# Kernel tuning notes

Measured on AMD Instinct MI355X. Metric: run time of the kernel, lower is better.

## Reference

```python
import jax, jax.numpy as jnp
import numpy as np
from jax import lax

T, D_IN, N = 8192, 1024, 1024


def setup_inputs() -> dict:
    key = jax.random.key(0)
    ks = jax.random.split(key, 8)
    s = 0.1  # truncated_normal stddev in original
    return {
        "x": jax.random.normal(ks[0], (T, D_IN), jnp.float32),
        # input projections (FullConnectLayer weights + biases)
        "Wx": jax.random.normal(ks[1], (D_IN, N), jnp.float32) * s,
        "bx": jnp.zeros((N,), jnp.float32),
        "Wu": jax.random.normal(ks[2], (D_IN, N), jnp.float32) * s,
        "bu": jnp.zeros((N,), jnp.float32),
        "Wr": jax.random.normal(ks[3], (D_IN, N), jnp.float32) * s,
        "br": jnp.zeros((N,), jnp.float32),
        # recurrent weights/biases
        "hW": jax.random.normal(ks[4], (N, N), jnp.float32) * s,
        "hUW": jax.random.normal(ks[5], (N, N), jnp.float32) * s,
        "hRW": jax.random.normal(ks[6], (N, N), jnp.float32) * s,
        "hB": jnp.zeros((N,), jnp.float32),
        "hUB": jnp.zeros((N,), jnp.float32),
        "hRB": jnp.zeros((N,), jnp.float32),
        # initial hidden state h (tf.Variable zeros [1, nNodes])
        "h0": jnp.zeros((1, N), jnp.float32),
    }


def reference(x, Wx, bx, Wu, bu, Wr, br, hW, hUW, hRW, hB, hUB, hRB, h0):
    # Precompute input-side gate projections for all timesteps (as original
    # does: xTransform/xUpdates/xResets are built once on the full sequence).
    xT = x @ Wx + bx  # [T, N] candidate input
    xU = x @ Wu + bu  # [T, N] update gate input
    xR = x @ Wr + br  # [T, N] reset gate input

    def step(h, xs):  # h: [N]
        xt, xu, xr = xs
        u = jax.nn.sigmoid(xu + h @ hUW + hUB)
        r = jax.nn.sigmoid(xr + h @ hRW + hRB)
        hc = jnp.tanh(xt + (r * h) @ hW + hB)
        # NOTE: faithful to original bug: (1-u)*hc + u*hc == hc
        h_new = (1.0 - u) * hc + u * hc
        return h_new, h_new

    _, hs = lax.scan(step, h0[0], (xT, xU, xR))
    return hs  # [T, N] == hStates.concat() since each state is [1, N]
```

## Files before the change

### kernel.cpp

```cpp
#include <hip/hip_runtime.h>
#include <hip/hip_bf16.h>
#include <math.h>

#define T_STEPS 8192
#define NN      1024
#define KWG     32
#define RT      512

typedef float f32x4 __attribute__((ext_vector_type(4)));

#define REP16(X) X(0) X(1) X(2) X(3) X(4) X(5) X(6) X(7) \
                 X(8) X(9) X(10) X(11) X(12) X(13) X(14) X(15)
#define REP8(X)  X(0) X(1) X(2) X(3) X(4) X(5) X(6) X(7)

__device__ __forceinline__ float fast_sigmoid(float z) {
    z = fminf(fmaxf(z, -30.f), 30.f);
    return 1.f / (1.f + __expf(-z));
}
__device__ __forceinline__ float fast_tanh(float x) {
    x = fminf(fmaxf(x, -9.f), 9.f);
    const float e = __expf(2.f * x);
    return (e - 1.f) / (e + 1.f);
}

__global__ __launch_bounds__(256) void gemm_bias(
    const float* __restrict__ A, const float* __restrict__ W,
    const float* __restrict__ bias, float* __restrict__ C)
{
    const int bn = blockIdx.x;
    const int bm = blockIdx.y;
    const int tid = threadIdx.x;

    __shared__ __align__(16) float As[16][68];
    __shared__ __align__(16) float Bs[16][68];

    const int row0 = bm * 64, col0 = bn * 64;
    const int tm = (tid >> 4) << 2;
    const int tn = (tid & 15) << 2;

    float acc[4][4] = {};

    for (int k0 = 0; k0 < 1024; k0 += 16) {
        {
            const int m = tid >> 2, kq = (tid & 3) << 2;
            const float4 v = *reinterpret_cast<const float4*>(&A[(size_t)(row0 + m) * 1024 + k0 + kq]);
            As[kq + 0][m] = v.x; As[kq + 1][m] = v.y; As[kq + 2][m] = v.z; As[kq + 3][m] = v.w;
            const int kk = tid >> 4, nq = (tid & 15) << 2;
            *reinterpret_cast<float4*>(&Bs[kk][nq]) =
                *reinterpret_cast<const float4*>(&W[(size_t)(k0 + kk) * 1024 + col0 + nq]);
        }
        __syncthreads();
#pragma unroll
        for (int k = 0; k < 16; ++k) {
            const float4 a4 = *reinterpret_cast<const float4*>(&As[k][tm]);
            const float4 b4 = *reinterpret_cast<const float4*>(&Bs[k][tn]);
            const float a[4] = {a4.x, a4.y, a4.z, a4.w};
            const float b[4] = {b4.x, b4.y, b4.z, b4.w};
#pragma unroll
            for (int i = 0; i < 4; ++i)
#pragma unroll
                for (int j = 0; j < 4; ++j) acc[i][j] += a[i] * b[j];
        }
        __syncthreads();
    }
#pragma unroll
    for (int i = 0; i < 4; ++i)
#pragma unroll
        for (int j = 0; j < 4; ++j)
            C[(size_t)(row0 + tm + i) * 1024 + col0 + tn + j] = acc[i][j] + bias[col0 + tn + j];
}

__global__ __launch_bounds__(RT, 1) void gru_rec(
    const float* __restrict__ xT, const float* __restrict__ xR,
    const float* __restrict__ hRW, const float* __restrict__ hW,
    const float* __restrict__ hRB, const float* __restrict__ hB,
    const float* __restrict__ h0, float* __restrict__ out,
    unsigned long long* __restrict__ P,
    unsigned long long* __restrict__ hbc)
{
    const int g = blockIdx.x;
    const int tid = threadIdx.x;
    const int lane = tid & 63;
    const int wave = tid >> 6;

    __shared__ __align__(16) float hsh[1088];
    __shared__ __align__(16) float rh[32];

    const int j = (wave << 2) | (lane >> 4);
    const int c = lane & 15;
    const bool leader1 = (c == 0);
    const int colj = g * 32 + j;

#define LD_W1(q) f32x4 w1_##q = { \
        hRW[(size_t)(c * 64 + 4 * q + 0) * NN + colj], \
        hRW[(size_t)(c * 64 + 4 * q + 1) * NN + colj], \
        hRW[(size_t)(c * 64 + 4 * q + 2) * NN + colj], \
        hRW[(size_t)(c * 64 + 4 * q + 3) * NN + colj] };
    REP16(LD_W1)

    const int n0 = tid, n1 = tid + RT;
    const int pi0 = n0 + (n0 >> 6) * 4, pi1 = n1 + (n1 >> 6) * 4;
#define LD_W2A(q) f32x4 w2a_##q = { \
        hW[(size_t)(g * 32 + 4 * q + 0) * NN + n0], \
        hW[(size_t)(g * 32 + 4 * q + 1) * NN + n0], \
        hW[(size_t)(g * 32 + 4 * q + 2) * NN + n0], \
        hW[(size_t)(g * 32 + 4 * q + 3) * NN + n0] };
    REP8(LD_W2A)
#define LD_W2B(q) f32x4 w2b_##q = { \
        hW[(size_t)(g * 32 + 4 * q + 0) * NN + n1], \
        hW[(size_t)(g * 32 + 4 * q + 1) * NN + n1], \
        hW[(size_t)(g * 32 + 4 * q + 2) * NN + n1], \
        hW[(size_t)(g * 32 + 4 * q + 3) * NN + n1] };
    REP8(LD_W2B)

#define PIN_W1(q)  asm volatile("" : "+v"(w1_##q));
#define PIN_W2A(q) asm volatile("" : "+v"(w2a_##q));
#define PIN_W2B(q) asm volatile("" : "+v"(w2b_##q));
    REP16(PIN_W1)
    REP8(PIN_W2A)
    REP8(PIN_W2B)

    const int jj = tid >> 4, cc = tid & 15;
    const int mjj = g * 32 + jj;
    const float hBo = hB[mjj];

    const int mj = colj;
    const int pij = mj + (mj >> 6) * 4;
    const float hRBj = hRB[mj];

    hsh[pi0] = h0[n0];
    hsh[pi1] = h0[n1];
    __syncthreads();

    float xr_n  = leader1   ? xR[mj]  : 0.f;
    float xto_n = (cc == 0) ? xT[mjj] : 0.f;

    for (int t = 0; t < T_STEPS; ++t) {
        const unsigned tag = (unsigned)(t + 1);
        unsigned long long* __restrict__ Pb = P   + (size_t)(t & 1) * KWG * NN;
        unsigned long long* __restrict__ Hb = hbc + (size_t)(t & 1) * NN;

        const float xr = xr_n, xto = xto_n;
        if (t + 1 < T_STEPS) {
            if (leader1) xr_n  = xR[(size_t)(t + 1) * NN + mj];
            if (cc == 0) xto_n = xT[(size_t)(t + 1) * NN + mjj];
        }

        f32x4 acc = {0.f, 0.f, 0.f, 0.f};
#define FMA_W1(q) { \
        const f32x4 hv = *reinterpret_cast<const f32x4*>(&hsh[c * 68 + 4 * q]); \
        acc += hv * w1_##q; }
        REP16(FMA_W1)
        float s = (acc.x + acc.y) + (acc.z + acc.w);
        s += __shfl_xor(s, 1); s += __shfl_xor(s, 2);
        s += __shfl_xor(s, 4); s += __shfl_xor(s, 8);
        if (leader1) rh[j] = fast_sigmoid(xr + hRBj + s) * hsh[pij];
        __syncthreads();

        f32x4 aa = {0.f, 0.f, 0.f, 0.f}, bb = {0.f, 0.f, 0.f, 0.f};
#define FMA_W2(q) { \
        const f32x4 rv = *reinterpret_cast<const f32x4*>(&rh[4 * q]); \
        aa += rv * w2a_##q; bb += rv * w2b_##q; }
        REP8(FMA_W2)
        const float p0 = (aa.x + aa.y) + (aa.z + aa.w);
        const float p1 = (bb.x + bb.y) + (bb.z + bb.w);
        __hip_atomic_store(&Pb[(size_t)g * NN + n0],
            ((unsigned long long)tag << 32) | (unsigned)__float_as_uint(p0),
            __ATOMIC_RELAXED, __HIP_MEMORY_SCOPE_AGENT);
        __hip_atomic_store(&Pb[(size_t)g * NN + n1],
            ((unsigned long long)tag << 32) | (unsigned)__float_as_uint(p1),
            __ATOMIC_RELAXED, __HIP_MEMORY_SCOPE_AGENT);

        float hn;
        {
            unsigned long long va = 0, vb = 0;
            bool fa = false, fb = false;
            do {
                if (!fa) { va = __hip_atomic_load(&Pb[(size_t)cc * NN + mjj],
                             __ATOMIC_RELAXED, __HIP_MEMORY_SCOPE_AGENT);
                           fa = ((unsigned)(va >> 32) == tag); }
                if (!fb) { vb = __hip_atomic_load(&Pb[(size_t)(cc + 16) * NN + mjj],
                             __ATOMIC_RELAXED, __HIP_MEMORY_SCOPE_AGENT);
                           fb = ((unsigned)(vb >> 32) == tag); }
            } while (!(fa && fb));
            float s2 = __uint_as_float((unsigned)va) + __uint_as_float((unsigned)vb);
            s2 += __shfl_xor(s2, 1); s2 += __shfl_xor(s2, 2);
            s2 += __shfl_xor(s2, 4); s2 += __shfl_xor(s2, 8);
            hn = fast_tanh(xto ? xto + s2 + hBo : s2 + hBo);
            hn = fast_tanh(__shfl(xto, (tid & ~15) & 63, 64) + s2 + hBo);
            if (cc == 0) {
                __hip_atomic_store(&Hb[mjj],
                    ((unsigned long long)tag << 32) | (unsigned)__float_as_uint(hn),
                    __ATOMIC_RELAXED, __HIP_MEMORY_SCOPE_AGENT);
            }
            if (cc == 1) out[(size_t)t * NN + mjj] = hn;
        }

        {
            unsigned long long ua = 0, ub = 0;
            bool fa = false, fb = false;
            do {
                if (!fa) { ua = __hip_atomic_load(&Hb[n0], __ATOMIC_RELAXED,
                             __HIP_MEMORY_SCOPE_AGENT);
                           fa = ((unsigned)(ua >> 32) == tag); }
                if (!fb) { ub = __hip_atomic_load(&Hb[n1], __ATOMIC_RELAXED,
                             __HIP_MEMORY_SCOPE_AGENT);
                           fb = ((unsigned)(ub >> 32) == tag); }
            } while (!(fa && fb));
            hsh[pi0] = __uint_as_float((unsigned)ua);
            hsh[pi1] = __uint_as_float((unsigned)ub);
        }
        __syncthreads();
    }
}

extern "C" void kernel_launch(void* const* d_in, const int* in_sizes, int n_in,
                              void* d_out, int out_size, void* d_ws, size_t ws_size,
                              hipStream_t stream) {
    const float* x   = (const float*)d_in[0];
    const float* Wx  = (const float*)d_in[1];
    const float* bx  = (const float*)d_in[2];
    const float* Wr  = (const float*)d_in[5];
    const float* br  = (const float*)d_in[6];
    const float* hW  = (const float*)d_in[7];
    const float* hRW = (const float*)d_in[9];
    const float* hB  = (const float*)d_in[10];
    const float* hRB = (const float*)d_in[12];
    const float* h0  = (const float*)d_in[13];
    float* out = (float*)d_out;

    char* ws = (char*)d_ws;
    float* xT = (float*)(ws);
    float* xR = (float*)(ws + 33554432);
    unsigned long long* P   = (unsigned long long*)(ws + 67108864);
    unsigned long long* hbc = (unsigned long long*)(ws + 67108864 + 524288);

    hipMemsetAsync(P, 0, (2 * KWG * NN + 2 * NN) * sizeof(unsigned long long), stream);

    gemm_bias<<<dim3(16, 128), 256, 0, stream>>>(x, Wx, bx, xT);
    gemm_bias<<<dim3(16, 128), 256, 0, stream>>>(x, Wr, br, xR);

    gru_rec<<<dim3(KWG), RT, 0, stream>>>(xT, xR, hRW, hW, hRB, hB, h0,
                                          out, P, hbc);
}
```

Measured before the change: 31.28 ms.

## Co-locate recurrent workgroups on one XCC and use non-coherent fast polling

Launches many workgroups and elects the 32 that land on one XCC (read from the hardware XCC id), so the per-step cross-workgroup exchange stays inside a single die's L2. Stores are written twice, once as a plain store and once as an agent-scope atomic, and polling first spins with sc0 loads before falling back to agent-scope atomic loads. The goal is to cut the latency of the per-timestep global handshake. It adds a startup election and barrier with a timeout, and depends on all 32 elected workgroups being resident at once. The fast path relies on cache-coherence behaviour that the code assumes rather than guarantees.

Measured after the change: 83.66 ms. 2.67x slower.

```diff
diff --git a/kernel.cpp b/kernel.cpp
--- a/kernel.cpp
+++ b/kernel.cpp
@@ -6,6 +6,8 @@
 #define NN      1024
 #define KWG     32
 #define RT      512
+#define NWG_LAUNCH 1024
+#define FAST_SPIN 24
 
 typedef float f32x4 __attribute__((ext_vector_type(4)));
 
@@ -21,6 +23,43 @@
     x = fminf(fmaxf(x, -9.f), 9.f);
     const float e = __expf(2.f * x);
     return (e - 1.f) / (e + 1.f);
+}
+
+__device__ __forceinline__ void st_2way(unsigned long long* p, unsigned long long v) {
+    asm volatile("global_store_dwordx2 %0, %1, off" :: "v"(p), "v"(v) : "memory");
+    __hip_atomic_store(p, v, __ATOMIC_RELAXED, __HIP_MEMORY_SCOPE_AGENT);
+}
+
+__device__ __forceinline__ bool poll2(const unsigned long long* pa,
+                                      const unsigned long long* pb,
+                                      unsigned tag, bool use_fast,
+                                      unsigned long long& va, unsigned long long& vb) {
+    bool fa = false, fb = false;
+    if (use_fast) {
+        for (int it = 0; it < FAST_SPIN; ++it) {
+            unsigned long long xa, xb;
+            asm volatile("global_load_dwordx2 %0, %2, off sc0\n\t"
+                         "global_load_dwordx2 %1, %3, off sc0\n\t"
+                         "s_waitcnt vmcnt(0)"
+                         : "=&v"(xa), "=&v"(xb) : "v"(pa), "v"(pb) : "memory");
+            if (!fa && (unsigned)(xa >> 32) == tag) { va = xa; fa = true; }
+            if (!fb && (unsigned)(xb >> 32) == tag) { vb = xb; fb = true; }
+            if (fa && fb) return true;
+        }
+    }
+    for (;;) {
+        if (!fa) {
+            const unsigned long long xa =
+                __hip_atomic_load(pa, __ATOMIC_RELAXED, __HIP_MEMORY_SCOPE_AGENT);
+            if ((unsigned)(xa >> 32) == tag) { va = xa; fa = true; }
+        }
+        if (!fb) {
+            const unsigned long long xb =
+                __hip_atomic_load(pb, __ATOMIC_RELAXED, __HIP_MEMORY_SCOPE_AGENT);
+            if ((unsigned)(xb >> 32) == tag) { vb = xb; fb = true; }
+        }
+        if (fa && fb) return false;
+    }
 }
 
 __global__ __launch_bounds__(256) void gemm_bias(
@@ -76,10 +115,29 @@
     const float* __restrict__ hRB, const float* __restrict__ hB,
     const float* __restrict__ h0, float* __restrict__ out,
     unsigned long long* __restrict__ P,
-    unsigned long long* __restrict__ hbc)
+    unsigned long long* __restrict__ hbc,
+    unsigned int* __restrict__ elect)
 {
-    const int g = blockIdx.x;
     const int tid = threadIdx.x;
+
+    __shared__ int s_g;
+    if (tid == 0) {
+        unsigned xcc;
+        asm volatile("s_getreg_b32 %0, hwreg(HW_REG_XCC_ID)" : "=s"(xcc));
+        xcc = (xcc & 0xfu) + 1u;
+        const unsigned old = atomicCAS(&elect[0], 0u, xcc);
+        const unsigned home = old ? old : xcc;
+        int slot = -1;
+        if (home == xcc) {
+            const unsigned s = atomicAdd(&elect[1], 1u);
+            if (s < KWG) slot = (int)s;
+        }
+        s_g = slot;
+    }
+    __syncthreads();
+    const int g = s_g;
+    if (g < 0) return;
+
     const int lane = tid & 63;
     const int wave = tid >> 6;
 
@@ -132,8 +190,18 @@
     hsh[pi1] = h0[n1];
     __syncthreads();
 
+    if (tid == 0) {
+        __hip_atomic_fetch_add(&elect[2], 1u, __ATOMIC_RELAXED, __HIP_MEMORY_SCOPE_AGENT);
+        const long long t0 = clock64();
+        while (__hip_atomic_load(&elect[2], __ATOMIC_RELAXED, __HIP_MEMORY_SCOPE_AGENT) < KWG
+               && (clock64() - t0) < (1LL << 22)) {}
+    }
+    __syncthreads();
+
     float xr_n  = leader1   ? xR[mj]  : 0.f;
     float xto_n = (cc == 0) ? xT[mjj] : 0.f;
+
+    bool fast1 = true, fast2 = true;
 
     for (int t = 0; t < T_STEPS; ++t) {
         const unsigned tag = (unsigned)(t + 1);
@@ -164,49 +232,32 @@
         REP8(FMA_W2)
         const float p0 = (aa.x + aa.y) + (aa.z + aa.w);
         const float p1 = (bb.x + bb.y) + (bb.z + bb.w);
-        __hip_atomic_store(&Pb[(size_t)g * NN + n0],
-            ((unsigned long long)tag << 32) | (unsigned)__float_as_uint(p0),
-            __ATOMIC_RELAXED, __HIP_MEMORY_SCOPE_AGENT);
-        __hip_atomic_store(&Pb[(size_t)g * NN + n1],
-            ((unsigned long long)tag << 32) | (unsigned)__float_as_uint(p1),
-            __ATOMIC_RELAXED, __HIP_MEMORY_SCOPE_AGENT);
-
-        float hn;
+        st_2way(&Pb[(size_t)g * NN + n0],
+                ((unsigned long long)tag << 32) | (unsigned)__float_as_uint(p0));
+        st_2way(&Pb[(size_t)g * NN + n1],
+                ((unsigned long long)tag << 32) | (unsigned)__float_as_uint(p1));
+
         {
             unsigned long long va = 0, vb = 0;
-            bool fa = false, fb = false;
-            do {
-                if (!fa) { va = __hip_atomic_load(&Pb[(size_t)cc * NN + mjj],
-                             __ATOMIC_RELAXED, __HIP_MEMORY_SCOPE_AGENT);
-                           fa = ((unsigned)(va >> 32) == tag); }
-                if (!fb) { vb = __hip_atomic_load(&Pb[(size_t)(cc + 16) * NN + mjj],
-                             __ATOMIC_RELAXED, __HIP_MEMORY_SCOPE_AGENT);
-                           fb = ((unsigned)(vb >> 32) == tag); }
-            } while (!(fa && fb));
+            const bool ff = poll2(&Pb[(size_t)cc * NN + mjj],
+                                  &Pb[(size_t)(cc + 16) * NN + mjj],
+                                  tag, fast1, va, vb);
+            fast1 = fast1 && ff;
             float s2 = __uint_as_float((unsigned)va) + __uint_as_float((unsigned)vb);
             s2 += __shfl_xor(s2, 1); s2 += __shfl_xor(s2, 2);
             s2 += __shfl_xor(s2, 4); s2 += __shfl_xor(s2, 8);
-            hn = fast_tanh(xto ? xto + s2 + hBo : s2 + hBo);
-            hn = fast_tanh(__shfl(xto, (tid & ~15) & 63, 64) + s2 + hBo);
             if (cc == 0) {
-                __hip_atomic_store(&Hb[mjj],
-                    ((unsigned long long)tag << 32) | (unsigned)__float_as_uint(hn),
-                    __ATOMIC_RELAXED, __HIP_MEMORY_SCOPE_AGENT);
+                const float hn = fast_tanh(xto + s2 + hBo);
+                st_2way(&Hb[mjj],
+                        ((unsigned long long)tag << 32) | (unsigned)__float_as_uint(hn));
+                out[(size_t)t * NN + mjj] = hn;
             }
-            if (cc == 1) out[(size_t)t * NN + mjj] = hn;
         }
 
         {
             unsigned long long ua = 0, ub = 0;
-            bool fa = false, fb = false;
-            do {
-                if (!fa) { ua = __hip_atomic_load(&Hb[n0], __ATOMIC_RELAXED,
-                             __HIP_MEMORY_SCOPE_AGENT);
-                           fa = ((unsigned)(ua >> 32) == tag); }
-                if (!fb) { ub = __hip_atomic_load(&Hb[n1], __ATOMIC_RELAXED,
-                             __HIP_MEMORY_SCOPE_AGENT);
-                           fb = ((unsigned)(ub >> 32) == tag); }
-            } while (!(fa && fb));
+            const bool ff = poll2(&Hb[n0], &Hb[n1], tag, fast2, ua, ub);
+            fast2 = fast2 && ff;
             hsh[pi0] = __uint_as_float((unsigned)ua);
             hsh[pi1] = __uint_as_float((unsigned)ub);
         }
@@ -232,14 +283,15 @@
     char* ws = (char*)d_ws;
     float* xT = (float*)(ws);
     float* xR = (float*)(ws + 33554432);
-    unsigned long long* P   = (unsigned long long*)(ws + 67108864);
-    unsigned long long* hbc = (unsigned long long*)(ws + 67108864 + 524288);
-
-    hipMemsetAsync(P, 0, (2 * KWG * NN + 2 * NN) * sizeof(unsigned long long), stream);
+    unsigned int* elect = (unsigned int*)(ws + 67108864);
+    unsigned long long* P   = (unsigned long long*)(ws + 67108864 + 4096);
+    unsigned long long* hbc = (unsigned long long*)(ws + 67108864 + 4096 + 524288);
+
+    hipMemsetAsync(ws + 67108864, 0, 4096 + 524288 + 16384, stream);
 
     gemm_bias<<<dim3(16, 128), 256, 0, stream>>>(x, Wx, bx, xT);
     gemm_bias<<<dim3(16, 128), 256, 0, stream>>>(x, Wr, br, xR);
 
-    gru_rec<<<dim3(KWG), RT, 0, stream>>>(xT, xR, hRW, hW, hRB, hB, h0,
-                                          out, P, hbc);
-}
+    gru_rec<<<dim3(NWG_LAUNCH), RT, 0, stream>>>(xT, xR, hRW, hW, hRB, hB, h0,
+                                                 out, P, hbc, elect);
+}
```

## Remove second grid-wide h broadcast by having every block reduce all partials redundantly

Applied to the files above, without the earlier changes.

Each block now gathers all 32 partial sums for the two hidden units each thread needs and applies tanh locally. This removes the separate hbc broadcast round and its second cross-block spin-wait per timestep. In exchange, global atomic-load traffic grows (32 loads per thread per step instead of 2) and the tanh is computed redundantly. The xT/xR prefetch for the next step is dropped in favour of direct loads at the current step.

After: 80.08 ms. 2.56x slower.

```diff
diff --git a/kernel.cpp b/kernel.cpp
--- a/kernel.cpp
+++ b/kernel.cpp
@@ -75,8 +75,7 @@
     const float* __restrict__ hRW, const float* __restrict__ hW,
     const float* __restrict__ hRB, const float* __restrict__ hB,
     const float* __restrict__ h0, float* __restrict__ out,
-    unsigned long long* __restrict__ P,
-    unsigned long long* __restrict__ hbc)
+    unsigned long long* __restrict__ P)
 {
     const int g = blockIdx.x;
     const int tid = threadIdx.x;
@@ -120,9 +119,8 @@
     REP8(PIN_W2A)
     REP8(PIN_W2B)
 
-    const int jj = tid >> 4, cc = tid & 15;
-    const int mjj = g * 32 + jj;
-    const float hBo = hB[mjj];
+    const float hB0 = hB[n0], hB1 = hB[n1];
+    const bool own0 = ((n0 >> 5) == g), own1 = ((n1 >> 5) == g);
 
     const int mj = colj;
     const int pij = mj + (mj >> 6) * 4;
@@ -132,19 +130,32 @@
     hsh[pi1] = h0[n1];
     __syncthreads();
 
-    float xr_n  = leader1   ? xR[mj]  : 0.f;
-    float xto_n = (cc == 0) ? xT[mjj] : 0.f;
+#define GATHER16(BASEPTR, SUMVAR, BIT) \
+    if (!(dmask & (BIT))) { \
+        unsigned long long v[16]; \
+        _Pragma("unroll") \
+        for (int q = 0; q < 16; ++q) \
+            v[q] = __hip_atomic_load((BASEPTR) + (size_t)q * NN, \
+                                     __ATOMIC_RELAXED, __HIP_MEMORY_SCOPE_AGENT); \
+        bool ok = true; \
+        _Pragma("unroll") \
+        for (int q = 0; q < 16; ++q) \
+            ok = ok && ((unsigned)(v[q] >> 32) == tag); \
+        if (ok) { \
+            float ssum = 0.f; \
+            _Pragma("unroll") \
+            for (int q = 0; q < 16; ++q) ssum += __uint_as_float((unsigned)v[q]); \
+            SUMVAR = ssum; dmask |= (BIT); \
+        } \
+    }
 
     for (int t = 0; t < T_STEPS; ++t) {
         const unsigned tag = (unsigned)(t + 1);
-        unsigned long long* __restrict__ Pb = P   + (size_t)(t & 1) * KWG * NN;
-        unsigned long long* __restrict__ Hb = hbc + (size_t)(t & 1) * NN;
-
-        const float xr = xr_n, xto = xto_n;
-        if (t + 1 < T_STEPS) {
-            if (leader1) xr_n  = xR[(size_t)(t + 1) * NN + mj];
-            if (cc == 0) xto_n = xT[(size_t)(t + 1) * NN + mjj];
-        }
+        unsigned long long* __restrict__ Pb = P + (size_t)(t & 1) * KWG * NN;
+
+        const float xt0 = xT[(size_t)t * NN + n0];
+        const float xt1 = xT[(size_t)t * NN + n1];
+        const float xr = leader1 ? xR[(size_t)t * NN + mj] : 0.f;
 
         f32x4 acc = {0.f, 0.f, 0.f, 0.f};
 #define FMA_W1(q) { \
@@ -171,45 +182,25 @@
             ((unsigned long long)tag << 32) | (unsigned)__float_as_uint(p1),
             __ATOMIC_RELAXED, __HIP_MEMORY_SCOPE_AGENT);
 
-        float hn;
-        {
-            unsigned long long va = 0, vb = 0;
-            bool fa = false, fb = false;
-            do {
-                if (!fa) { va = __hip_atomic_load(&Pb[(size_t)cc * NN + mjj],
-                             __ATOMIC_RELAXED, __HIP_MEMORY_SCOPE_AGENT);
-                           fa = ((unsigned)(va >> 32) == tag); }
-                if (!fb) { vb = __hip_atomic_load(&Pb[(size_t)(cc + 16) * NN + mjj],
-                             __ATOMIC_RELAXED, __HIP_MEMORY_SCOPE_AGENT);
-                           fb = ((unsigned)(vb >> 32) == tag); }
-            } while (!(fa && fb));
-            float s2 = __uint_as_float((unsigned)va) + __uint_as_float((unsigned)vb);
-            s2 += __shfl_xor(s2, 1); s2 += __shfl_xor(s2, 2);
-            s2 += __shfl_xor(s2, 4); s2 += __shfl_xor(s2, 8);
-            hn = fast_tanh(xto ? xto + s2 + hBo : s2 + hBo);
-            hn = fast_tanh(__shfl(xto, (tid & ~15) & 63, 64) + s2 + hBo);
-            if (cc == 0) {
-                __hip_atomic_store(&Hb[mjj],
-                    ((unsigned long long)tag << 32) | (unsigned)__float_as_uint(hn),
-                    __ATOMIC_RELAXED, __HIP_MEMORY_SCOPE_AGENT);
-            }
-            if (cc == 1) out[(size_t)t * NN + mjj] = hn;
-        }
-
-        {
-            unsigned long long ua = 0, ub = 0;
-            bool fa = false, fb = false;
-            do {
-                if (!fa) { ua = __hip_atomic_load(&Hb[n0], __ATOMIC_RELAXED,
-                             __HIP_MEMORY_SCOPE_AGENT);
-                           fa = ((unsigned)(ua >> 32) == tag); }
-                if (!fb) { ub = __hip_atomic_load(&Hb[n1], __ATOMIC_RELAXED,
-                             __HIP_MEMORY_SCOPE_AGENT);
-                           fb = ((unsigned)(ub >> 32) == tag); }
-            } while (!(fa && fb));
-            hsh[pi0] = __uint_as_float((unsigned)ua);
-            hsh[pi1] = __uint_as_float((unsigned)ub);
-        }
+        unsigned dmask = 0;
+        float s0a = 0.f, s0b = 0.f, s1a = 0.f, s1b = 0.f;
+        const unsigned long long* Pb0  = Pb + n0;
+        const unsigned long long* Pb0h = Pb + (size_t)16 * NN + n0;
+        const unsigned long long* Pb1  = Pb + n1;
+        const unsigned long long* Pb1h = Pb + (size_t)16 * NN + n1;
+        do {
+            GATHER16(Pb0,  s0a, 1u)
+            GATHER16(Pb0h, s0b, 2u)
+            GATHER16(Pb1,  s1a, 4u)
+            GATHER16(Pb1h, s1b, 8u)
+        } while (dmask != 15u);
+
+        const float hn0 = fast_tanh(xt0 + (s0a + s0b) + hB0);
+        const float hn1 = fast_tanh(xt1 + (s1a + s1b) + hB1);
+        hsh[pi0] = hn0;
+        hsh[pi1] = hn1;
+        if (own0) out[(size_t)t * NN + n0] = hn0;
+        if (own1) out[(size_t)t * NN + n1] = hn1;
         __syncthreads();
     }
 }
@@ -232,14 +223,12 @@
     char* ws = (char*)d_ws;
     float* xT = (float*)(ws);
     float* xR = (float*)(ws + 33554432);
-    unsigned long long* P   = (unsigned long long*)(ws + 67108864);
-    unsigned long long* hbc = (unsigned long long*)(ws + 67108864 + 524288);
-
-    hipMemsetAsync(P, 0, (2 * KWG * NN + 2 * NN) * sizeof(unsigned long long), stream);
+    unsigned long long* P = (unsigned long long*)(ws + 67108864);
+
+    hipMemsetAsync(P, 0, (size_t)2 * KWG * NN * sizeof(unsigned long long), stream);
 
     gemm_bias<<<dim3(16, 128), 256, 0, stream>>>(x, Wx, bx, xT);
     gemm_bias<<<dim3(16, 128), 256, 0, stream>>>(x, Wr, br, xR);
 
-    gru_rec<<<dim3(KWG), RT, 0, stream>>>(xT, xR, hRW, hW, hRB, hB, h0,
-                                          out, P, hbc);
-}
+    gru_rec<<<dim3(KWG), RT, 0, stream>>>(xT, xR, hRW, hW, hRB, hB, h0, out, P);
+}
```
